# Kernel tuning notes

Hardware: AMD Instinct MI355X
Metric: run time of the kernel (lower is better)

The kernel has to match this reference:

```python
import jax, jax.numpy as jnp
import numpy as np

# ---- constants (from init_kwargs / Config) ----
C = 10            # number of classes
P = 128           # fixed prototype capacity per class (masked)
GAMMA = 0.1
B_CONST = 10.0    # b
TAO = 1.0
BETA = 1.0
LAMBDA = 0.1
THRESHOLD = 40.0
EPS = 1e-6        # nn.PairwiseDistance eps (added to the difference)


def setup_inputs() -> dict:
    key = jax.random.key(0)
    k1, k2 = jax.random.split(key)
    features = jax.random.normal(k1, (8192, 512), dtype=jnp.float32)
    labels = jax.random.randint(k2, (8192,), 0, C, dtype=jnp.int32)
    return {"features": features, "labels": labels}


def _assign_prototypes(features, labels):
    """Sequential prototype assignment (faithful to assign_prototype).
    Fixed-capacity store: protos [C,P,D], counts [C,P], nproto [C]."""
    D = features.shape[1]
    protos = jnp.zeros((C, P, D), features.dtype)
    counts = jnp.zeros((C, P), jnp.int32)
    nproto = jnp.zeros((C,), jnp.int32)

    def step(carry, xs):
        protos, counts, nproto = carry
        f, l = xs
        row = protos[l]                       # [P, D]
        cnt = counts[l]                       # [P]
        n = nproto[l]
        valid = jnp.arange(P) < n
        d2 = jnp.sum((f[None, :] - row + EPS) ** 2, axis=-1)
        d2m = jnp.where(valid, d2, jnp.inf)
        idx = jnp.argmin(d2m)
        dmin = jnp.sqrt(d2m[idx])
        do_update = (n > 0) & (dmin < THRESHOLD)
        # running-mean update of closest prototype
        c = cnt[idx].astype(f.dtype)
        new_val = (row[idx] * c + f) / (c + 1.0)
        app_idx = jnp.minimum(n, P - 1)       # append slot (clamped; never hit with these settings)
        tgt_idx = jnp.where(do_update, idx, app_idx)
        tgt_val = jnp.where(do_update, new_val, f)
        tgt_cnt = jnp.where(do_update, cnt[idx] + 1, 1)
        row = row.at[tgt_idx].set(tgt_val)
        cnt = cnt.at[tgt_idx].set(tgt_cnt)
        n = jnp.where(do_update, n, jnp.minimum(n + 1, P))
        protos = protos.at[l].set(row)
        counts = counts.at[l].set(cnt)
        nproto = nproto.at[l].set(n)
        return (protos, counts, nproto), None

    (protos, counts, nproto), _ = jax.lax.scan(step, (protos, counts, nproto), (features, labels))
    return protos, nproto


def _forward(features, labels):
    # assign_prototype uses tensor(features).detach() -> stop_gradient
    protos, nproto = _assign_prototypes(jax.lax.stop_gradient(features), labels)
    B, D = features.shape
    flat = protos.reshape(C * P, D)
    valid = (jnp.arange(P)[None, :] < nproto[:, None]).reshape(C * P)

    # squared PairwiseDistance with eps added to the difference:
    # sum((f - p + eps)^2) = |f|^2 + |p|^2 - 2 f.p + 2*eps*(sum f - sum p) + D*eps^2
    f2 = jnp.sum(features ** 2, axis=-1)          # [B]
    p2 = jnp.sum(flat ** 2, axis=-1)              # [C*P]
    sf = jnp.sum(features, axis=-1)
    sp = jnp.sum(flat, axis=-1)
    d2 = (f2[:, None] + p2[None, :] - 2.0 * (features @ flat.T)
          + 2.0 * EPS * (sf[:, None] - sp[None, :]) + D * EPS * EPS)
    d2 = jnp.maximum(d2, 0.0)                     # [B, C*P]

    # dce loss: probability = 1e-6 + sum_label exp(-g d^2) / sum_all exp(-g d^2)
    expv = jnp.where(valid[None, :], jnp.exp(-GAMMA * d2), 0.0)
    per_class = expv.reshape(B, C, P).sum(-1)     # [B, C]
    one = per_class.sum(-1)                       # [B]
    num = jnp.take_along_axis(per_class, labels[:, None].astype(jnp.int32), axis=1)[:, 0]
    prob = 1e-6 + jnp.where(one > 0.0, num / one, one)
    dce_loss = jnp.sum(-jnp.log(prob))

    # pairwise loss: per sample, per existing class, min distance
    d2c = jnp.where(valid[None, :], d2, jnp.inf).reshape(B, C, P).min(-1)
    dmin = jnp.sqrt(d2c)                          # [B, C]
    sign = jnp.where(labels[:, None] == jnp.arange(C)[None, :], 1.0, -1.0)
    z = B_CONST - (TAO - dmin) * sign
    g = jnp.where(z > 10.0, z, jax.nn.softplus(BETA * z) / BETA)
    exists = nproto > 0                           # only classes present in all_prototypes
    pw_loss = jnp.sum(jnp.where(exists[None, :], g, 0.0))

    return dce_loss + LAMBDA * pw_loss


def reference(features, labels):
    return _forward(features, labels)
```

## Files before the change

kernel.cpp:

```cpp
#include <hip/hip_runtime.h>
#include <math.h>

#define NC 10
#define NP 128
#define ND 512
#define GAMMA  0.1f
#define BCONST 10.0f
#define TAO    1.0f
#define LAMBDA 0.1f
#define THR2   1600.0f
#define FEPS   1e-6f
#define NLDS   12
#define CH     32
#define MAXCH  256
#define IMAX   0x7FFFFFFF

__device__ __forceinline__ float allred64(float v) {
#pragma unroll
  for (int m = 1; m < 64; m <<= 1) v += __shfl_xor(v, m, 64);
  return v;
}

__global__ __launch_bounds__(256)
void ord_kernel(const int* __restrict__ labels, int B,
                int* __restrict__ order, int* __restrict__ cls_base,
                int* __restrict__ cls_cnt, int* __restrict__ fail_pos,
                float* __restrict__ out)
{
  __shared__ int lab[8192];
  __shared__ int cnts[256][NC + 1];
  __shared__ int tot_s[NC], base_s[NC];
  const int t = threadIdx.x;

  const int4* lp = (const int4*)labels;
  for (int i = t; i < (B >> 2); i += 256) {
    int4 v = lp[i];
    lab[i*4+0] = v.x; lab[i*4+1] = v.y; lab[i*4+2] = v.z; lab[i*4+3] = v.w;
  }
  for (int i = (B & ~3) + t; i < B; i += 256) lab[i] = labels[i];
  __syncthreads();

  const int segsz = (B + 255) >> 8;
  const int s0 = t * segsz, s1 = min(s0 + segsz, B);

  int loc[NC];
#pragma unroll
  for (int c = 0; c < NC; ++c) loc[c] = 0;
  for (int i = s0; i < s1; ++i) {
    int l = lab[i];
#pragma unroll
    for (int c = 0; c < NC; ++c) loc[c] += (l == c) ? 1 : 0;
  }
#pragma unroll
  for (int c = 0; c < NC; ++c) cnts[t][c] = loc[c];
  __syncthreads();

#pragma unroll
  for (int s = 1; s < 256; s <<= 1) {
    int v[NC];
#pragma unroll
    for (int c = 0; c < NC; ++c) v[c] = (t >= s) ? cnts[t - s][c] : 0;
    __syncthreads();
#pragma unroll
    for (int c = 0; c < NC; ++c) cnts[t][c] += v[c];
    __syncthreads();
  }

  if (t == 0) {
    int b = 0;
    for (int c = 0; c < NC; ++c) {
      int tc = cnts[255][c];
      base_s[c] = b; tot_s[c] = tc;
      cls_base[c] = b; cls_cnt[c] = tc; fail_pos[c] = IMAX;
      b += tc;
    }
    out[0] = 0.f;
  }
  __syncthreads();

  int pos[NC];
#pragma unroll
  for (int c = 0; c < NC; ++c) pos[c] = base_s[c] + cnts[t][c] - loc[c];
  for (int i = s0; i < s1; ++i) {
    int l = lab[i];
#pragma unroll
    for (int c = 0; c < NC; ++c)
      if (l == c) order[pos[c]++] = i;
  }
}

__global__ __launch_bounds__(64)
void chunksum_kernel(const float* __restrict__ feats, const int* __restrict__ order,
                     const int* __restrict__ cls_base, const int* __restrict__ cls_cnt,
                     float* __restrict__ chunksum)
{
  const int c = blockIdx.x / MAXCH, g = blockIdx.x % MAXCH;
  const int cnt = cls_cnt[c];
  const int nch = (cnt + CH - 1) / CH;
  if (g >= nch) return;
  const int base = cls_base[c], lane = threadIdx.x;
  const int k0 = g * CH, k1 = min(k0 + CH, cnt);
  int myidx = (lane < CH && k0 + lane < cnt) ? order[base + k0 + lane] : 0;

  float S[8] = {0, 0, 0, 0, 0, 0, 0, 0};
  int k = k0;
  for (; k + 4 <= k1; k += 4) {
    float4 A[4], Bv[4];
#pragma unroll
    for (int j = 0; j < 4; ++j) {
      int idx = __shfl(myidx, k + j - k0, 64);
      const float4* fp = (const float4*)(feats + (size_t)idx * ND + lane * 8);
      A[j] = fp[0]; Bv[j] = fp[1];
    }
#pragma unroll
    for (int j = 0; j < 4; ++j) {
      S[0]+=A[j].x; S[1]+=A[j].y; S[2]+=A[j].z; S[3]+=A[j].w;
      S[4]+=Bv[j].x; S[5]+=Bv[j].y; S[6]+=Bv[j].z; S[7]+=Bv[j].w;
    }
  }
  for (; k < k1; ++k) {
    int idx = __shfl(myidx, k - k0, 64);
    const float4* fp = (const float4*)(feats + (size_t)idx * ND + lane * 8);
    float4 a = fp[0], b = fp[1];
    S[0]+=a.x; S[1]+=a.y; S[2]+=a.z; S[3]+=a.w;
    S[4]+=b.x; S[5]+=b.y; S[6]+=b.z; S[7]+=b.w;
  }
  float4* cp = (float4*)(chunksum + ((size_t)c * MAXCH + g) * ND + lane * 8);
  cp[0] = make_float4(S[0], S[1], S[2], S[3]);
  cp[1] = make_float4(S[4], S[5], S[6], S[7]);
}

__global__ __launch_bounds__(256)
void scanfin_kernel(const int* __restrict__ cls_cnt,
                    float* __restrict__ chunksum, float* __restrict__ gproto,
                    float* __restrict__ p2s, float* __restrict__ sps,
                    int* __restrict__ nproto_g)
{
  __shared__ float red[8];
  const int c = blockIdx.x, t = threadIdx.x;
  const int cnt = cls_cnt[c];
  if (cnt == 0) { if (t == 0) nproto_g[c] = 0; return; }
  const int nch = (cnt + CH - 1) / CH;

  float* colA = chunksum + (size_t)c * MAXCH * ND + t;
  float* colB = colA + 256;
  float runA = 0.f, runB = 0.f;
  int g = 0;
  for (; g + 4 <= nch; g += 4) {
    float a0 = colA[(size_t)(g+0)*ND], b0 = colB[(size_t)(g+0)*ND];
    float a1 = colA[(size_t)(g+1)*ND], b1 = colB[(size_t)(g+1)*ND];
    float a2 = colA[(size_t)(g+2)*ND], b2 = colB[(size_t)(g+2)*ND];
    float a3 = colA[(size_t)(g+3)*ND], b3 = colB[(size_t)(g+3)*ND];
    colA[(size_t)(g+0)*ND] = runA;            colB[(size_t)(g+0)*ND] = runB;
    runA += a0; runB += b0;
    colA[(size_t)(g+1)*ND] = runA;            colB[(size_t)(g+1)*ND] = runB;
    runA += a1; runB += b1;
    colA[(size_t)(g+2)*ND] = runA;            colB[(size_t)(g+2)*ND] = runB;
    runA += a2; runB += b2;
    colA[(size_t)(g+3)*ND] = runA;            colB[(size_t)(g+3)*ND] = runB;
    runA += a3; runB += b3;
  }
  for (; g < nch; ++g) {
    float a = colA[(size_t)g*ND], b = colB[(size_t)g*ND];
    colA[(size_t)g*ND] = runA; colB[(size_t)g*ND] = runB;
    runA += a; runB += b;
  }

  float inv = 1.f / (float)cnt;
  float pA = runA * inv, pB = runB * inv;
  gproto[(size_t)c * NP * ND + t]       = pA;
  gproto[(size_t)c * NP * ND + t + 256] = pB;

  float P2p = pA * pA + pB * pB;
  float SPp = pA + pB;
  float P2 = allred64(P2p), SP = allred64(SPp);
  const int lane = t & 63, wid = t >> 6;
  if (lane == 0) { red[wid] = P2; red[4 + wid] = SP; }
  __syncthreads();
  if (t == 0) {
    p2s[c * NP] = red[0] + red[1] + red[2] + red[3];
    sps[c * NP] = red[4] + red[5] + red[6] + red[7];
    nproto_g[c] = 1;
  }
}

__global__ __launch_bounds__(64)
void verify_kernel(const float* __restrict__ feats, const int* __restrict__ order,
                   const int* __restrict__ cls_base, const int* __restrict__ cls_cnt,
                   const float* __restrict__ chunksum, int* __restrict__ fail_pos)
{
  const int c = blockIdx.x / MAXCH, g = blockIdx.x % MAXCH;
  const int cnt = cls_cnt[c];
  const int nch = (cnt + CH - 1) / CH;
  if (g >= nch) return;
  const int base = cls_base[c], lane = threadIdx.x;
  const int k0 = g * CH, k1 = min(k0 + CH, cnt);
  int myidx = (lane < CH && k0 + lane < cnt) ? order[base + k0 + lane] : 0;

  const float4* cp = (const float4*)(chunksum + ((size_t)c * MAXCH + g) * ND + lane * 8);
  float4 a = cp[0], b = cp[1];
  float S[8] = {a.x, a.y, a.z, a.w, b.x, b.y, b.z, b.w};

  int k = k0;
  for (; k + 4 <= k1; k += 4) {
    float4 A[4], Bv[4];
#pragma unroll
    for (int j = 0; j < 4; ++j) {
      int idx = __shfl(myidx, k + j - k0, 64);
      const float4* fp = (const float4*)(feats + (size_t)idx * ND + lane * 8);
      A[j] = fp[0]; Bv[j] = fp[1];
    }
#pragma unroll
    for (int j = 0; j < 4; ++j) {
      int kk = k + j;
      float f[8] = {A[j].x, A[j].y, A[j].z, A[j].w, Bv[j].x, Bv[j].y, Bv[j].z, Bv[j].w};
      if (kk > 0) {
        float inv = 1.f / (float)kk;
        float part = 0.f;
#pragma unroll
        for (int e = 0; e < 8; ++e) { float d = f[e] - S[e] * inv + FEPS; part += d * d; }
        float d2 = allred64(part);
        if (!(d2 < THR2) && lane == 0) atomicMin(&fail_pos[c], kk);
      }
#pragma unroll
      for (int e = 0; e < 8; ++e) S[e] += f[e];
    }
  }
  for (; k < k1; ++k) {
    int idx = __shfl(myidx, k - k0, 64);
    const float4* fp = (const float4*)(feats + (size_t)idx * ND + lane * 8);
    float4 fa = fp[0], fb = fp[1];
    float f[8] = {fa.x, fa.y, fa.z, fa.w, fb.x, fb.y, fb.z, fb.w};
    if (k > 0) {
      float inv = 1.f / (float)k;
      float part = 0.f;
#pragma unroll
      for (int e = 0; e < 8; ++e) { float d = f[e] - S[e] * inv + FEPS; part += d * d; }
      float d2 = allred64(part);
      if (!(d2 < THR2) && lane == 0) atomicMin(&fail_pos[c], k);
    }
#pragma unroll
    for (int e = 0; e < 8; ++e) S[e] += f[e];
  }
}

__global__ __launch_bounds__(64)
void fallback_kernel(const float* __restrict__ feats, const int* __restrict__ order,
                     const int* __restrict__ cls_base, const int* __restrict__ cls_cnt,
                     const int* __restrict__ fail_pos,
                     float* __restrict__ gproto, float* __restrict__ p2s,
                     float* __restrict__ sps, int* __restrict__ nproto_g)
{
  const int c = blockIdx.x;
  if (fail_pos[c] == IMAX) return;

  __shared__ float ls_proto[NLDS][ND];
  __shared__ int   ls_cnt[NP];
  const int lane = threadIdx.x;
  const int base = cls_base[c], cnt = cls_cnt[c];

  float p0[8];
  int cnt0 = 0, n = 0;
  float fA[8], fB[8], fC[8];

  auto LOADF = [&](float (&buf)[8], int m) {
    int idx = order[base + m];
    const float4* fp = (const float4*)(feats + (size_t)idx * ND + lane * 8);
    float4 a = fp[0], b = fp[1];
    buf[0]=a.x; buf[1]=a.y; buf[2]=a.z; buf[3]=a.w;
    buf[4]=b.x; buf[5]=b.y; buf[6]=b.z; buf[7]=b.w;
  };

  auto STEP = [&](float (&f)[8]) {
    float best = 3.4e38f;
    int bidx = 0;
    if (n > 0) {
      float part = 0.f;
#pragma unroll
      for (int e = 0; e < 8; ++e) { float d = f[e] - p0[e] + FEPS; part += d * d; }
      best = allred64(part);
      for (int j = 1; j < n; ++j) {
        float pj[8];
        if (j <= NLDS) {
          const float4* pp = (const float4*)(&ls_proto[j-1][lane*8]);
          float4 a = pp[0], b = pp[1];
          pj[0]=a.x; pj[1]=a.y; pj[2]=a.z; pj[3]=a.w;
          pj[4]=b.x; pj[5]=b.y; pj[6]=b.z; pj[7]=b.w;
        } else {
          const float4* pp = (const float4*)(gproto + ((size_t)c*NP + j)*ND + lane*8);
          float4 a = pp[0], b = pp[1];
          pj[0]=a.x; pj[1]=a.y; pj[2]=a.z; pj[3]=a.w;
          pj[4]=b.x; pj[5]=b.y; pj[6]=b.z; pj[7]=b.w;
        }
        float part2 = 0.f;
#pragma unroll
        for (int e = 0; e < 8; ++e) { float d = f[e] - pj[e] + FEPS; part2 += d * d; }
        float tot = allred64(part2);
        if (tot < best) { best = tot; bidx = j; }
      }
    }
    if (n > 0 && best < THR2) {
      if (bidx == 0) {
        float cc = (float)cnt0, inv = 1.f / (cc + 1.f);
#pragma unroll
        for (int e = 0; e < 8; ++e) p0[e] = (p0[e]*cc + f[e]) * inv;
        cnt0++;
      } else {
        int ci = ls_cnt[bidx];
        float cc = (float)ci, inv = 1.f / (cc + 1.f);
        if (bidx <= NLDS) {
          float* row = &ls_proto[bidx-1][lane*8];
#pragma unroll
          for (int e = 0; e < 8; ++e) row[e] = (row[e]*cc + f[e]) * inv;
        } else {
          float* row = gproto + ((size_t)c*NP + bidx)*ND + lane*8;
#pragma unroll
          for (int e = 0; e < 8; ++e) row[e] = (row[e]*cc + f[e]) * inv;
        }
        if (lane == 0) ls_cnt[bidx] = ci + 1;
      }
    } else {
      int app = min(n, NP - 1);
      if (app == 0) {
#pragma unroll
        for (int e = 0; e < 8; ++e) p0[e] = f[e];
        cnt0 = 1;
      } else if (app <= NLDS) {
        float* row = &ls_proto[app-1][lane*8];
#pragma unroll
        for (int e = 0; e < 8; ++e) row[e] = f[e];
        if (lane == 0) ls_cnt[app] = 1;
      } else {
        float* row = gproto + ((size_t)c*NP + app)*ND + lane*8;
#pragma unroll
        for (int e = 0; e < 8; ++e) row[e] = f[e];
        if (lane == 0) ls_cnt[app] = 1;
      }
      n = min(n + 1, NP);
    }
  };

  if (cnt > 0) LOADF(fA, 0);
  if (cnt > 1) LOADF(fB, 1);
  if (cnt > 2) LOADF(fC, 2);
  int m = 0;
  while (m < cnt) {
    STEP(fA); ++m; if (m + 2 < cnt) LOADF(fA, m + 2);
    if (m >= cnt) break;
    STEP(fB); ++m; if (m + 2 < cnt) LOADF(fB, m + 2);
    if (m >= cnt) break;
    STEP(fC); ++m; if (m + 2 < cnt) LOADF(fC, m + 2);
  }

  for (int j = 0; j < n; ++j) {
    float pj[8];
    if (j == 0) {
#pragma unroll
      for (int e = 0; e < 8; ++e) pj[e] = p0[e];
    } else if (j <= NLDS) {
      const float4* pp = (const float4*)(&ls_proto[j-1][lane*8]);
      float4 a = pp[0], b = pp[1];
      pj[0]=a.x; pj[1]=a.y; pj[2]=a.z; pj[3]=a.w;
      pj[4]=b.x; pj[5]=b.y; pj[6]=b.z; pj[7]=b.w;
    } else {
      const float4* pp = (const float4*)(gproto + ((size_t)c*NP + j)*ND + lane*8);
      float4 a = pp[0], b = pp[1];
      pj[0]=a.x; pj[1]=a.y; pj[2]=a.z; pj[3]=a.w;
      pj[4]=b.x; pj[5]=b.y; pj[6]=b.z; pj[7]=b.w;
    }
    float4* gp = (float4*)(gproto + ((size_t)c*NP + j)*ND + lane*8);
    gp[0] = make_float4(pj[0], pj[1], pj[2], pj[3]);
    gp[1] = make_float4(pj[4], pj[5], pj[6], pj[7]);
    float P2p = 0.f, SPp = 0.f;
#pragma unroll
    for (int e = 0; e < 8; ++e) { P2p += pj[e]*pj[e]; SPp += pj[e]; }
    float P2 = allred64(P2p), SP = allred64(SPp);
    if (lane == 0) { p2s[c*NP + j] = P2; sps[c*NP + j] = SP; }
  }
  if (lane == 0) nproto_g[c] = n;
}

__global__ __launch_bounds__(256)
void loss_kernel(const float* __restrict__ feats, const int* __restrict__ labels, int B,
                 const float* __restrict__ gproto, const float* __restrict__ p2s,
                 const float* __restrict__ sps, const int* __restrict__ nproto_g,
                 float* __restrict__ out)
{
  __shared__ float bsum[4];
  const int lane = threadIdx.x & 63;
  const int wid  = threadIdx.x >> 6;
  const int gw   = blockIdx.x * 4 + wid;
  const int nw   = gridDim.x * 4;

  int np[NC];
#pragma unroll
  for (int cc = 0; cc < NC; ++cc) np[cc] = nproto_g[cc];

  float acc = 0.f;
  for (int b = gw; b < B; b += nw) {
    const float4* fp = (const float4*)(feats + (size_t)b * ND + lane * 8);
    float4 a4 = fp[0], b4 = fp[1];
    float f[8] = {a4.x, a4.y, a4.z, a4.w, b4.x, b4.y, b4.z, b4.w};
    float f2p = 0.f, sfp = 0.f;
#pragma unroll
    for (int e = 0; e < 8; ++e) { f2p += f[e]*f[e]; sfp += f[e]; }
    float f2 = allred64(f2p);
    float sf = allred64(sfp);
    int lab = labels[b];

    float one = 0.f, num = 0.f, pw = 0.f;
    for (int cc = 0; cc < NC; ++cc) {
      int nn = np[cc];
      if (nn <= 0) continue;
      float sume = 0.f, bestd2 = 3.4e38f;
      for (int j = 0; j < nn; ++j) {
        const float4* pp = (const float4*)(gproto + ((size_t)cc*NP + j)*ND + lane*8);
        float4 pa = pp[0], pb = pp[1];
        float dp = f[0]*pa.x + f[1]*pa.y + f[2]*pa.z + f[3]*pa.w
                 + f[4]*pb.x + f[5]*pb.y + f[6]*pb.z + f[7]*pb.w;
        float dot = allred64(dp);
        float d2 = f2 + p2s[cc*NP + j] - 2.f*dot
                 + 2.f*FEPS*(sf - sps[cc*NP + j]) + (float)ND*FEPS*FEPS;
        d2 = fmaxf(d2, 0.f);
        sume  += expf(-GAMMA * d2);
        bestd2 = fminf(bestd2, d2);
      }
      one += sume;
      if (cc == lab) num = sume;
      float dmin = sqrtf(bestd2);
      float sign = (cc == lab) ? 1.f : -1.f;
      float z = BCONST - (TAO - dmin) * sign;
      float g = (z > 10.f) ? z : log1pf(expf(z));
      pw += g;
    }
    float prob = 1e-6f + ((one > 0.f) ? num / one : one);
    acc += -logf(prob) + LAMBDA * pw;
  }

  if (lane == 0) bsum[wid] = acc;
  __syncthreads();
  if (threadIdx.x == 0) atomicAdd(out, bsum[0] + bsum[1] + bsum[2] + bsum[3]);
}

extern "C" void kernel_launch(void* const* d_in, const int* in_sizes, int n_in,
                              void* d_out, int out_size, void* d_ws, size_t ws_size,
                              hipStream_t stream) {
  const float* feats  = (const float*)d_in[0];
  const int*   labels = (const int*)d_in[1];
  int B = in_sizes[0] / ND;

  float* gproto   = (float*)d_ws;
  float* p2s      = gproto + (size_t)NC * NP * ND;
  float* sps      = p2s + NC * NP;
  float* chunksum = sps + NC * NP;
  int*   nproto_g = (int*)(chunksum + (size_t)NC * MAXCH * ND);
  int*   order    = nproto_g + NC;
  int*   cls_base = order + B;
  int*   cls_cnt  = cls_base + NC;
  int*   fail_pos = cls_cnt + NC;

  hipLaunchKernelGGL(ord_kernel, dim3(1), dim3(256), 0, stream,
                     labels, B, order, cls_base, cls_cnt, fail_pos, (float*)d_out);
  hipLaunchKernelGGL(chunksum_kernel, dim3(NC * MAXCH), dim3(64), 0, stream,
                     feats, order, cls_base, cls_cnt, chunksum);
  hipLaunchKernelGGL(scanfin_kernel, dim3(NC), dim3(256), 0, stream,
                     cls_cnt, chunksum, gproto, p2s, sps, nproto_g);
  hipLaunchKernelGGL(verify_kernel, dim3(NC * MAXCH), dim3(64), 0, stream,
                     feats, order, cls_base, cls_cnt, chunksum, fail_pos);
  hipLaunchKernelGGL(fallback_kernel, dim3(NC), dim3(64), 0, stream,
                     feats, order, cls_base, cls_cnt, fail_pos,
                     gproto, p2s, sps, nproto_g);
  hipLaunchKernelGGL(loss_kernel, dim3(2048), dim3(256), 0, stream,
                     feats, labels, B, gproto, p2s, sps, nproto_g, (float*)d_out);
}
```

Before: 92.67 us.

## Fuse chunk sum, prefix scan and verify into one kernel with flag-based decoupled lookback

Merges the chunksum, scanfin and verify kernels into a single kernel. Each block publishes its chunk sum with a release flag, then waits on the flags of all earlier chunks in its class and sums their partials to get its prefix. The last chunk of each class also writes the class mean prototype and its norms. The goal is to remove two kernel launches and the separate scan pass. In exchange, later chunks do O(g) re-reads of earlier chunk sums, and the spin-waits rely on earlier blocks being scheduled first to avoid deadlock.

New measurement: 115.3 us. +24.4%, slower.

```diff
diff --git a/kernel.cpp b/kernel.cpp
--- a/kernel.cpp
+++ b/kernel.cpp
@@ -25,12 +25,17 @@
 void ord_kernel(const int* __restrict__ labels, int B,
                 int* __restrict__ order, int* __restrict__ cls_base,
                 int* __restrict__ cls_cnt, int* __restrict__ fail_pos,
+                int* __restrict__ flags, int* __restrict__ nproto_g,
                 float* __restrict__ out)
 {
   __shared__ int lab[8192];
   __shared__ int cnts[256][NC + 1];
-  __shared__ int tot_s[NC], base_s[NC];
+  __shared__ int base_s[NC];
   const int t = threadIdx.x;
+
+  for (int i = t; i < NC * MAXCH; i += 256) flags[i] = 0;
+  if (t < NC) { fail_pos[t] = IMAX; nproto_g[t] = 0; }
+  if (t == 0) out[0] = 0.f;
 
   const int4* lp = (const int4*)labels;
   for (int i = t; i < (B >> 2); i += 256) {
@@ -70,11 +75,10 @@
     int b = 0;
     for (int c = 0; c < NC; ++c) {
       int tc = cnts[255][c];
-      base_s[c] = b; tot_s[c] = tc;
-      cls_base[c] = b; cls_cnt[c] = tc; fail_pos[c] = IMAX;
+      base_s[c] = b;
+      cls_base[c] = b; cls_cnt[c] = tc;
       b += tc;
     }
-    out[0] = 0.f;
   }
   __syncthreads();
 
@@ -90,9 +94,12 @@
 }
 
 __global__ __launch_bounds__(64)
-void chunksum_kernel(const float* __restrict__ feats, const int* __restrict__ order,
-                     const int* __restrict__ cls_base, const int* __restrict__ cls_cnt,
-                     float* __restrict__ chunksum)
+void sumverify_kernel(const float* __restrict__ feats, const int* __restrict__ order,
+                      const int* __restrict__ cls_base, const int* __restrict__ cls_cnt,
+                      float* __restrict__ chunksum, int* __restrict__ flags,
+                      int* __restrict__ fail_pos,
+                      float* __restrict__ gproto, float* __restrict__ p2s,
+                      float* __restrict__ sps, int* __restrict__ nproto_g)
 {
   const int c = blockIdx.x / MAXCH, g = blockIdx.x % MAXCH;
   const int cnt = cls_cnt[c];
@@ -103,144 +110,124 @@
   int myidx = (lane < CH && k0 + lane < cnt) ? order[base + k0 + lane] : 0;
 
   float S[8] = {0, 0, 0, 0, 0, 0, 0, 0};
-  int k = k0;
-  for (; k + 4 <= k1; k += 4) {
-    float4 A[4], Bv[4];
-#pragma unroll
-    for (int j = 0; j < 4; ++j) {
-      int idx = __shfl(myidx, k + j - k0, 64);
+  {
+    int k = k0;
+    for (; k + 4 <= k1; k += 4) {
+      float4 A[4], Bv[4];
+#pragma unroll
+      for (int j = 0; j < 4; ++j) {
+        int idx = __shfl(myidx, k + j - k0, 64);
+        const float4* fp = (const float4*)(feats + (size_t)idx * ND + lane * 8);
+        A[j] = fp[0]; Bv[j] = fp[1];
+      }
+#pragma unroll
+      for (int j = 0; j < 4; ++j) {
+        S[0]+=A[j].x; S[1]+=A[j].y; S[2]+=A[j].z; S[3]+=A[j].w;
+        S[4]+=Bv[j].x; S[5]+=Bv[j].y; S[6]+=Bv[j].z; S[7]+=Bv[j].w;
+      }
+    }
+    for (; k < k1; ++k) {
+      int idx = __shfl(myidx, k - k0, 64);
       const float4* fp = (const float4*)(feats + (size_t)idx * ND + lane * 8);
-      A[j] = fp[0]; Bv[j] = fp[1];
-    }
-#pragma unroll
-    for (int j = 0; j < 4; ++j) {
-      S[0]+=A[j].x; S[1]+=A[j].y; S[2]+=A[j].z; S[3]+=A[j].w;
-      S[4]+=Bv[j].x; S[5]+=Bv[j].y; S[6]+=Bv[j].z; S[7]+=Bv[j].w;
-    }
-  }
-  for (; k < k1; ++k) {
-    int idx = __shfl(myidx, k - k0, 64);
-    const float4* fp = (const float4*)(feats + (size_t)idx * ND + lane * 8);
-    float4 a = fp[0], b = fp[1];
-    S[0]+=a.x; S[1]+=a.y; S[2]+=a.z; S[3]+=a.w;
-    S[4]+=b.x; S[5]+=b.y; S[6]+=b.z; S[7]+=b.w;
+      float4 a = fp[0], b = fp[1];
+      S[0]+=a.x; S[1]+=a.y; S[2]+=a.z; S[3]+=a.w;
+      S[4]+=b.x; S[5]+=b.y; S[6]+=b.z; S[7]+=b.w;
+    }
   }
   float4* cp = (float4*)(chunksum + ((size_t)c * MAXCH + g) * ND + lane * 8);
   cp[0] = make_float4(S[0], S[1], S[2], S[3]);
   cp[1] = make_float4(S[4], S[5], S[6], S[7]);
-}
-
-__global__ __launch_bounds__(256)
-void scanfin_kernel(const int* __restrict__ cls_cnt,
-                    float* __restrict__ chunksum, float* __restrict__ gproto,
-                    float* __restrict__ p2s, float* __restrict__ sps,
-                    int* __restrict__ nproto_g)
-{
-  __shared__ float red[8];
-  const int c = blockIdx.x, t = threadIdx.x;
-  const int cnt = cls_cnt[c];
-  if (cnt == 0) { if (t == 0) nproto_g[c] = 0; return; }
-  const int nch = (cnt + CH - 1) / CH;
-
-  float* colA = chunksum + (size_t)c * MAXCH * ND + t;
-  float* colB = colA + 256;
-  float runA = 0.f, runB = 0.f;
-  int g = 0;
-  for (; g + 4 <= nch; g += 4) {
-    float a0 = colA[(size_t)(g+0)*ND], b0 = colB[(size_t)(g+0)*ND];
-    float a1 = colA[(size_t)(g+1)*ND], b1 = colB[(size_t)(g+1)*ND];
-    float a2 = colA[(size_t)(g+2)*ND], b2 = colB[(size_t)(g+2)*ND];
-    float a3 = colA[(size_t)(g+3)*ND], b3 = colB[(size_t)(g+3)*ND];
-    colA[(size_t)(g+0)*ND] = runA;            colB[(size_t)(g+0)*ND] = runB;
-    runA += a0; runB += b0;
-    colA[(size_t)(g+1)*ND] = runA;            colB[(size_t)(g+1)*ND] = runB;
-    runA += a1; runB += b1;
-    colA[(size_t)(g+2)*ND] = runA;            colB[(size_t)(g+2)*ND] = runB;
-    runA += a2; runB += b2;
-    colA[(size_t)(g+3)*ND] = runA;            colB[(size_t)(g+3)*ND] = runB;
-    runA += a3; runB += b3;
-  }
-  for (; g < nch; ++g) {
-    float a = colA[(size_t)g*ND], b = colB[(size_t)g*ND];
-    colA[(size_t)g*ND] = runA; colB[(size_t)g*ND] = runB;
-    runA += a; runB += b;
-  }
-
-  float inv = 1.f / (float)cnt;
-  float pA = runA * inv, pB = runB * inv;
-  gproto[(size_t)c * NP * ND + t]       = pA;
-  gproto[(size_t)c * NP * ND + t + 256] = pB;
-
-  float P2p = pA * pA + pB * pB;
-  float SPp = pA + pB;
-  float P2 = allred64(P2p), SP = allred64(SPp);
-  const int lane = t & 63, wid = t >> 6;
-  if (lane == 0) { red[wid] = P2; red[4 + wid] = SP; }
-  __syncthreads();
-  if (t == 0) {
-    p2s[c * NP] = red[0] + red[1] + red[2] + red[3];
-    sps[c * NP] = red[4] + red[5] + red[6] + red[7];
-    nproto_g[c] = 1;
-  }
-}
-
-__global__ __launch_bounds__(64)
-void verify_kernel(const float* __restrict__ feats, const int* __restrict__ order,
-                   const int* __restrict__ cls_base, const int* __restrict__ cls_cnt,
-                   const float* __restrict__ chunksum, int* __restrict__ fail_pos)
-{
-  const int c = blockIdx.x / MAXCH, g = blockIdx.x % MAXCH;
-  const int cnt = cls_cnt[c];
-  const int nch = (cnt + CH - 1) / CH;
-  if (g >= nch) return;
-  const int base = cls_base[c], lane = threadIdx.x;
-  const int k0 = g * CH, k1 = min(k0 + CH, cnt);
-  int myidx = (lane < CH && k0 + lane < cnt) ? order[base + k0 + lane] : 0;
-
-  const float4* cp = (const float4*)(chunksum + ((size_t)c * MAXCH + g) * ND + lane * 8);
-  float4 a = cp[0], b = cp[1];
-  float S[8] = {a.x, a.y, a.z, a.w, b.x, b.y, b.z, b.w};
-
-  int k = k0;
-  for (; k + 4 <= k1; k += 4) {
-    float4 A[4], Bv[4];
-#pragma unroll
-    for (int j = 0; j < 4; ++j) {
-      int idx = __shfl(myidx, k + j - k0, 64);
+  __threadfence();
+  if (lane == 0)
+    __hip_atomic_store(&flags[c * MAXCH + g], 1, __ATOMIC_RELEASE, __HIP_MEMORY_SCOPE_AGENT);
+
+  for (int j = lane; j < g; j += 64)
+    while (__hip_atomic_load(&flags[c * MAXCH + j], __ATOMIC_ACQUIRE,
+                             __HIP_MEMORY_SCOPE_AGENT) == 0) { }
+  __threadfence();
+
+  float P[8] = {0, 0, 0, 0, 0, 0, 0, 0};
+  {
+    const float* cbase = chunksum + (size_t)c * MAXCH * ND + lane * 8;
+    int j = 0;
+    for (; j + 4 <= g; j += 4) {
+      float4 A[4], Bv[4];
+#pragma unroll
+      for (int q = 0; q < 4; ++q) {
+        const float4* pp = (const float4*)(cbase + (size_t)(j + q) * ND);
+        A[q] = pp[0]; Bv[q] = pp[1];
+      }
+#pragma unroll
+      for (int q = 0; q < 4; ++q) {
+        P[0]+=A[q].x; P[1]+=A[q].y; P[2]+=A[q].z; P[3]+=A[q].w;
+        P[4]+=Bv[q].x; P[5]+=Bv[q].y; P[6]+=Bv[q].z; P[7]+=Bv[q].w;
+      }
+    }
+    for (; j < g; ++j) {
+      const float4* pp = (const float4*)(cbase + (size_t)j * ND);
+      float4 a = pp[0], b = pp[1];
+      P[0]+=a.x; P[1]+=a.y; P[2]+=a.z; P[3]+=a.w;
+      P[4]+=b.x; P[5]+=b.y; P[6]+=b.z; P[7]+=b.w;
+    }
+  }
+
+  {
+    int k = k0;
+    for (; k + 4 <= k1; k += 4) {
+      float4 A[4], Bv[4];
+#pragma unroll
+      for (int j = 0; j < 4; ++j) {
+        int idx = __shfl(myidx, k + j - k0, 64);
+        const float4* fp = (const float4*)(feats + (size_t)idx * ND + lane * 8);
+        A[j] = fp[0]; Bv[j] = fp[1];
+      }
+#pragma unroll
+      for (int j = 0; j < 4; ++j) {
+        int kk = k + j;
+        float f[8] = {A[j].x, A[j].y, A[j].z, A[j].w, Bv[j].x, Bv[j].y, Bv[j].z, Bv[j].w};
+        if (kk > 0) {
+          float inv = 1.f / (float)kk;
+          float part = 0.f;
+#pragma unroll
+          for (int e = 0; e < 8; ++e) { float d = f[e] - P[e] * inv + FEPS; part += d * d; }
+          float d2 = allred64(part);
+          if (!(d2 < THR2) && lane == 0) atomicMin(&fail_pos[c], kk);
+        }
+#pragma unroll
+        for (int e = 0; e < 8; ++e) P[e] += f[e];
+      }
+    }
+    for (; k < k1; ++k) {
+      int idx = __shfl(myidx, k - k0, 64);
       const float4* fp = (const float4*)(feats + (size_t)idx * ND + lane * 8);
-      A[j] = fp[0]; Bv[j] = fp[1];
-    }
-#pragma unroll
-    for (int j = 0; j < 4; ++j) {
-      int kk = k + j;
-      float f[8] = {A[j].x, A[j].y, A[j].z, A[j].w, Bv[j].x, Bv[j].y, Bv[j].z, Bv[j].w};
-      if (kk > 0) {
-        float inv = 1.f / (float)kk;
+      float4 fa = fp[0], fb = fp[1];
+      float f[8] = {fa.x, fa.y, fa.z, fa.w, fb.x, fb.y, fb.z, fb.w};
+      if (k > 0) {
+        float inv = 1.f / (float)k;
         float part = 0.f;
 #pragma unroll
-        for (int e = 0; e < 8; ++e) { float d = f[e] - S[e] * inv + FEPS; part += d * d; }
+        for (int e = 0; e < 8; ++e) { float d = f[e] - P[e] * inv + FEPS; part += d * d; }
         float d2 = allred64(part);
-        if (!(d2 < THR2) && lane == 0) atomicMin(&fail_pos[c], kk);
-      }
-#pragma unroll
-      for (int e = 0; e < 8; ++e) S[e] += f[e];
-    }
-  }
-  for (; k < k1; ++k) {
-    int idx = __shfl(myidx, k - k0, 64);
-    const float4* fp = (const float4*)(feats + (size_t)idx * ND + lane * 8);
-    float4 fa = fp[0], fb = fp[1];
-    float f[8] = {fa.x, fa.y, fa.z, fa.w, fb.x, fb.y, fb.z, fb.w};
-    if (k > 0) {
-      float inv = 1.f / (float)k;
-      float part = 0.f;
-#pragma unroll
-      for (int e = 0; e < 8; ++e) { float d = f[e] - S[e] * inv + FEPS; part += d * d; }
-      float d2 = allred64(part);
-      if (!(d2 < THR2) && lane == 0) atomicMin(&fail_pos[c], k);
-    }
-#pragma unroll
-    for (int e = 0; e < 8; ++e) S[e] += f[e];
+        if (!(d2 < THR2) && lane == 0) atomicMin(&fail_pos[c], k);
+      }
+#pragma unroll
+      for (int e = 0; e < 8; ++e) P[e] += f[e];
+    }
+  }
+
+  if (g == nch - 1) {
+    float inv = 1.f / (float)cnt;
+    float p[8];
+#pragma unroll
+    for (int e = 0; e < 8; ++e) p[e] = P[e] * inv;
+    float4* gp = (float4*)(gproto + (size_t)c * NP * ND + lane * 8);
+    gp[0] = make_float4(p[0], p[1], p[2], p[3]);
+    gp[1] = make_float4(p[4], p[5], p[6], p[7]);
+    float P2p = 0.f, SPp = 0.f;
+#pragma unroll
+    for (int e = 0; e < 8; ++e) { P2p += p[e]*p[e]; SPp += p[e]; }
+    float P2 = allred64(P2p), SP = allred64(SPp);
+    if (lane == 0) { p2s[c*NP] = P2; sps[c*NP] = SP; nproto_g[c] = 1; }
   }
 }
 
@@ -458,15 +445,14 @@
   int*   cls_base = order + B;
   int*   cls_cnt  = cls_base + NC;
   int*   fail_pos = cls_cnt + NC;
+  int*   flags    = fail_pos + NC;
 
   hipLaunchKernelGGL(ord_kernel, dim3(1), dim3(256), 0, stream,
-                     labels, B, order, cls_base, cls_cnt, fail_pos, (float*)d_out);
-  hipLaunchKernelGGL(chunksum_kernel, dim3(NC * MAXCH), dim3(64), 0, stream,
-                     feats, order, cls_base, cls_cnt, chunksum);
-  hipLaunchKernelGGL(scanfin_kernel, dim3(NC), dim3(256), 0, stream,
-                     cls_cnt, chunksum, gproto, p2s, sps, nproto_g);
-  hipLaunchKernelGGL(verify_kernel, dim3(NC * MAXCH), dim3(64), 0, stream,
-                     feats, order, cls_base, cls_cnt, chunksum, fail_pos);
+                     labels, B, order, cls_base, cls_cnt, fail_pos, flags,
+                     nproto_g, (float*)d_out);
+  hipLaunchKernelGGL(sumverify_kernel, dim3(NC * MAXCH), dim3(64), 0, stream,
+                     feats, order, cls_base, cls_cnt, chunksum, flags,
+                     fail_pos, gproto, p2s, sps, nproto_g);
   hipLaunchKernelGGL(fallback_kernel, dim3(NC), dim3(64), 0, stream,
                      feats, order, cls_base, cls_cnt, fail_pos,
                      gproto, p2s, sps, nproto_g);
```
